# Performance work log

Hardware: AMD Instinct MI355X
Metric: run time of the kernel (lower is better)

The kernel has to match this reference:

```python
import jax, jax.numpy as jnp
import numpy as np
import math

EPS = 1e-7
STRIDES = (8, 16, 32)
ANCHOR_TABLE = np.array([[[12,16],[19,36],[40,28]],
                         [[36,75],[76,55],[72,146]],
                         [[142,110],[192,243],[459,401]]], dtype=np.float32)
OBJ_SCALE = (4.0, 1.0, 0.4)
B, A, C = 32, 3, 80
GRIDS = ((80, 80), (40, 40), (20, 20))
NTGT = (6000, 4000, 2000)
W_BOX, W_OBJ, W_CLS = 0.05, 0.7, 0.3


def bce_mean(logits, targets):
    # numerically-stable BCEWithLogits, mean reduction (pos_weight=1)
    return jnp.mean(jnp.maximum(logits, 0) - logits * targets
                    + jnp.log1p(jnp.exp(-jnp.abs(logits))))


def calculate_ciou(b1, b2):
    # boxes in xycwh; convert to xyxy
    def xyxy(b):
        cx, cy, w, h = b[..., 0], b[..., 1], b[..., 2], b[..., 3]
        return cx - w / 2, cy - h / 2, cx + w / 2, cy + h / 2
    x1a, y1a, x2a, y2a = xyxy(b1)
    x1b, y1b, x2b, y2b = xyxy(b2)
    iw = jnp.clip(jnp.minimum(x2a, x2b) - jnp.maximum(x1a, x1b), 0)
    ih = jnp.clip(jnp.minimum(y2a, y2b) - jnp.maximum(y1a, y1b), 0)
    inter = iw * ih
    union = (x2a - x1a) * (y2a - y1a) + (x2b - x1b) * (y2b - y1b) - inter
    iou = inter / (union + EPS)
    cw = jnp.maximum(x2a, x2b) - jnp.minimum(x1a, x1b)
    ch = jnp.maximum(y2a, y2b) - jnp.minimum(y1a, y1b)
    diag = cw ** 2 + ch ** 2 + EPS
    cent = ((x1a + x2a) / 2 - (x1b + x2b) / 2) ** 2 + ((y1a + y2a) / 2 - (y1b + y2b) / 2) ** 2
    at = jnp.arctan((x2a - x1a) / (y2a - y1a + EPS)) - jnp.arctan((x2b - x1b) / (y2b - y1b + EPS))
    v = (4.0 / math.pi ** 2) * at ** 2
    alpha = v / (v - iou + 1 + EPS)
    return iou - (cent / diag + v * alpha)


def setup_inputs() -> dict:
    key = jax.random.key(0)
    inp = {}
    for i in range(3):
        h, w = GRIDS[i]
        n = NTGT[i]
        ks = jax.random.split(jax.random.fold_in(key, i), 10)
        inp[f'box{i}'] = jax.random.normal(ks[0], (B, A, h, w, 4), jnp.float32)
        inp[f'cnf{i}'] = jax.random.normal(ks[1], (B, A, h, w, 1), jnp.float32)
        inp[f'cls{i}'] = jax.random.normal(ks[2], (B, A, h, w, C), jnp.float32)
        inp[f'b{i}'] = jax.random.randint(ks[3], (n,), 0, B, jnp.int32)
        a = jax.random.randint(ks[4], (n,), 0, A, jnp.int32)
        inp[f'a{i}'] = a
        inp[f'gy{i}'] = jax.random.randint(ks[5], (n,), 0, h, jnp.int32)
        inp[f'gx{i}'] = jax.random.randint(ks[6], (n,), 0, w, jnp.int32)
        inp[f'tcls{i}'] = jax.random.randint(ks[7], (n,), 0, C, jnp.int32)
        txy = jax.random.uniform(ks[8], (n, 2), jnp.float32) * 2.0 - 0.5   # grid_xy - grid_index
        twh = jax.random.uniform(ks[9], (n, 2), jnp.float32) * 7.5 + 0.5   # wh in grid units
        inp[f'tbox{i}'] = jnp.concatenate([txy, twh], axis=1)
        anc_tab = jnp.asarray(ANCHOR_TABLE[i] / STRIDES[i])                # [3,2]
        inp[f'anc{i}'] = anc_tab[a]                                        # per-target anchor wh
    return inp


def _scale_loss(pbox, pcnf, pcls, b, a, gy, gx, tbox, tcls, anc, obj_scale):
    pred = jnp.concatenate([pbox, pcnf, pcls], axis=-1)          # [B,A,H,W,5+C]
    p = pred[b, a, gy, gx]                                       # [N,5+C] gather
    pxy = jax.nn.sigmoid(p[:, :2]) * 2.0 - 0.5
    pwh = (jax.nn.sigmoid(p[:, 2:4]) * 2.0) ** 2 * anc
    pred_box = jnp.concatenate([pxy, pwh], axis=1)
    iou = calculate_ciou(pred_box, tbox)                         # [N]
    lbox = jnp.mean(1.0 - iou)
    tobj = jnp.zeros(pred.shape[:4], dtype=pred.dtype)
    tobj = tobj.at[b, a, gy, gx].set(jax.lax.stop_gradient(jnp.clip(iou, 0)))
    tcls_oh = jax.nn.one_hot(tcls, C, dtype=p.dtype)
    lcls = bce_mean(p[:, 5:], tcls_oh)
    lobj = bce_mean(pred[..., 4], tobj) * obj_scale
    return lbox, lobj, lcls


def reference(box0, cnf0, cls0, tbox0, anc0,
              box1, cnf1, cls1, tbox1, anc1,
              box2, cnf2, cls2, tbox2, anc2,
              b0, a0, gy0, gx0, tcls0,
              b1, a1, gy1, gx1, tcls1,
              b2, a2, gy2, gx2, tcls2):
    floats = [(box0, cnf0, cls0, tbox0, anc0),
              (box1, cnf1, cls1, tbox1, anc1),
              (box2, cnf2, cls2, tbox2, anc2)]
    ints = [(b0, a0, gy0, gx0, tcls0),
            (b1, a1, gy1, gx1, tcls1),
            (b2, a2, gy2, gx2, tcls2)]
    lbox = lobj = lcls = jnp.float32(0.0)
    for i in range(3):
        pbox, pcnf, pcls, tbox, anc = floats[i]
        b, a, gy, gx, tcls = ints[i]
        lb, lo, lc = _scale_loss(pbox, pcnf, pcls, b, a, gy, gx, tbox, tcls, anc, OBJ_SCALE[i])
        lbox, lobj, lcls = lbox + lb, lobj + lo, lcls + lc
    return jnp.stack([lbox * W_BOX * B, lobj * W_OBJ * B, lcls * W_CLS * B])
```

## Files before the change

### kernel.cpp

```cpp
#include <hip/hip_runtime.h>
#include <math.h>

#define EPSF 1e-7f
#define AA 3
#define CC 80
#define FOUR_OVER_PI2 0.4052847345693511f

__device__ __forceinline__ float sigmoidf_(float x) { return 1.0f / (1.0f + expf(-x)); }

__device__ __forceinline__ float bcef_(float x, float t) {
    return fmaxf(x, 0.0f) - x * t + log1pf(expf(-fabsf(x)));
}

__device__ __forceinline__ void block_reduce_add2(double v0, double v1, double* d0, double* d1) {
    __shared__ double s0[8], s1[8];
    const int lane = threadIdx.x & 63;
    const int wid  = threadIdx.x >> 6;
    #pragma unroll
    for (int off = 32; off > 0; off >>= 1) {
        v0 += __shfl_down(v0, off);
        v1 += __shfl_down(v1, off);
    }
    if (lane == 0) { s0[wid] = v0; s1[wid] = v1; }
    __syncthreads();
    if (threadIdx.x == 0) {
        const int nw = blockDim.x >> 6;
        double a = 0.0, b = 0.0;
        for (int w = 0; w < nw; ++w) { a += s0[w]; b += s1[w]; }
        atomicAdd(d0, a);
        atomicAdd(d1, b);
    }
}

__device__ __forceinline__ void block_reduce_add1(double v0, double* d0) {
    __shared__ double s0[8];
    const int lane = threadIdx.x & 63;
    const int wid  = threadIdx.x >> 6;
    #pragma unroll
    for (int off = 32; off > 0; off >>= 1) v0 += __shfl_down(v0, off);
    if (lane == 0) s0[wid] = v0;
    __syncthreads();
    if (threadIdx.x == 0) {
        const int nw = blockDim.x >> 6;
        double a = 0.0;
        for (int w = 0; w < nw; ++w) a += s0[w];
        atomicAdd(d0, a);
    }
}

__global__ __launch_bounds__(256) void target_kernel(
    const float* __restrict__ box, const float* __restrict__ cls,
    const int* __restrict__ tb, const int* __restrict__ ta,
    const int* __restrict__ tgy, const int* __restrict__ tgx,
    const int* __restrict__ ttc,
    const float* __restrict__ tbox, const float* __restrict__ anc,
    unsigned long long* __restrict__ tobj,
    double* __restrict__ accBox, double* __restrict__ accCls,
    int N, int H, int W)
{
    const int j = blockIdx.x * blockDim.x + threadIdx.x;
    float lb = 0.0f, lc = 0.0f;
    if (j < N) {
        const int b = tb[j], a = ta[j], gy = tgy[j], gx = tgx[j], tc = ttc[j];
        const long long cell = ((long long)((b * AA + a) * H + gy)) * W + gx;

        const float* bp = box + cell * 4;
        const float bx = bp[0], by = bp[1], bw = bp[2], bh = bp[3];

        const float px = sigmoidf_(bx) * 2.0f - 0.5f;
        const float py = sigmoidf_(by) * 2.0f - 0.5f;
        const float sw = sigmoidf_(bw) * 2.0f;
        const float sh = sigmoidf_(bh) * 2.0f;
        const float pw = sw * sw * anc[j * 2 + 0];
        const float ph = sh * sh * anc[j * 2 + 1];

        const float tx = tbox[j * 4 + 0], ty = tbox[j * 4 + 1];
        const float tw = tbox[j * 4 + 2], th = tbox[j * 4 + 3];

        const float x1a = px - pw * 0.5f, y1a = py - ph * 0.5f;
        const float x2a = px + pw * 0.5f, y2a = py + ph * 0.5f;
        const float x1b = tx - tw * 0.5f, y1b = ty - th * 0.5f;
        const float x2b = tx + tw * 0.5f, y2b = ty + th * 0.5f;

        const float iw = fmaxf(fminf(x2a, x2b) - fmaxf(x1a, x1b), 0.0f);
        const float ih = fmaxf(fminf(y2a, y2b) - fmaxf(y1a, y1b), 0.0f);
        const float inter = iw * ih;
        const float uni = (x2a - x1a) * (y2a - y1a) + (x2b - x1b) * (y2b - y1b) - inter;
        const float iou = inter / (uni + EPSF);
        const float cw = fmaxf(x2a, x2b) - fminf(x1a, x1b);
        const float ch = fmaxf(y2a, y2b) - fminf(y1a, y1b);
        const float diag = cw * cw + ch * ch + EPSF;
        const float dcx = (x1a + x2a) * 0.5f - (x1b + x2b) * 0.5f;
        const float dcy = (y1a + y2a) * 0.5f - (y1b + y2b) * 0.5f;
        const float cent = dcx * dcx + dcy * dcy;
        const float at = atanf((x2a - x1a) / ((y2a - y1a) + EPSF))
                       - atanf((x2b - x1b) / ((y2b - y1b) + EPSF));
        const float v = FOUR_OVER_PI2 * at * at;
        const float alpha = v / (v - iou + 1.0f + EPSF);
        const float ciou = iou - (cent / diag + v * alpha);

        lb = 1.0f - ciou;

        const float ioc = fmaxf(ciou, 0.0f);
        const unsigned long long pk =
            ((unsigned long long)(unsigned)(j + 1) << 32) |
            (unsigned long long)__float_as_uint(ioc);
        atomicMax(tobj + cell, pk);

        const float* cp = cls + cell * CC;
        float s = 0.0f;
        #pragma unroll 8
        for (int c = 0; c < CC; ++c) {
            const float x = cp[c];
            const float t = (c == tc) ? 1.0f : 0.0f;
            s += bcef_(x, t);
        }
        lc = s;
    }
    block_reduce_add2((double)lb, (double)lc, accBox, accCls);
}

__global__ __launch_bounds__(256) void obj_kernel(
    const float* __restrict__ cnf,
    const unsigned long long* __restrict__ tobj,
    double* __restrict__ accObj, int n4)
{
    const int stride = gridDim.x * blockDim.x;
    double s = 0.0;
    for (int idx = blockIdx.x * blockDim.x + threadIdx.x; idx < n4; idx += stride) {
        const float4 x4 = ((const float4*)cnf)[idx];
        const unsigned long long* tp = tobj + (long long)idx * 4;
        float xs[4] = {x4.x, x4.y, x4.z, x4.w};
        float ps = 0.0f;
        #pragma unroll
        for (int k = 0; k < 4; ++k) {
            const unsigned long long pk = tp[k];
            const float t = __uint_as_float((unsigned)(pk & 0xFFFFFFFFull));
            ps += bcef_(xs[k], t);
        }
        s += (double)ps;
    }
    block_reduce_add1(s, accObj);
}

__global__ void finalize_kernel(const double* __restrict__ acc, float* __restrict__ out) {
    if (threadIdx.x == 0 && blockIdx.x == 0) {
        const double lbox = acc[0] / 6000.0 + acc[1] / 4000.0 + acc[2] / 2000.0;
        const double lobj = (acc[3] / 614400.0) * 4.0
                          + (acc[4] / 153600.0) * 1.0
                          + (acc[5] /  38400.0) * 0.4;
        const double lcls = acc[6] / 480000.0 + acc[7] / 320000.0 + acc[8] / 160000.0;
        out[0] = (float)(lbox * 0.05 * 32.0);
        out[1] = (float)(lobj * 0.7 * 32.0);
        out[2] = (float)(lcls * 0.3 * 32.0);
    }
}

extern "C" void kernel_launch(void* const* d_in, const int* in_sizes, int n_in,
                              void* d_out, int out_size, void* d_ws, size_t ws_size,
                              hipStream_t stream) {
    const int NS[3]    = {6000, 4000, 2000};
    const int HS[3]    = {80, 40, 20};
    const int CELLS[3] = {32 * AA * 80 * 80, 32 * AA * 40 * 40, 32 * AA * 20 * 20};

    double* acc = (double*)d_ws;
    unsigned long long* tobj0 = (unsigned long long*)((char*)d_ws + 128);
    unsigned long long* tobj1 = tobj0 + CELLS[0];
    unsigned long long* tobj2 = tobj1 + CELLS[1];
    unsigned long long* tobjs[3] = {tobj0, tobj1, tobj2};

    const size_t zero_bytes = 128 + (size_t)(CELLS[0] + CELLS[1] + CELLS[2]) * 8;
    hipMemsetAsync(d_ws, 0, zero_bytes, stream);

    for (int i = 0; i < 3; ++i) {
        const int base = i * 10;
        const float* box  = (const float*)d_in[base + 0];
        const int*   b    = (const int*)  d_in[base + 3];
        const int*   a    = (const int*)  d_in[base + 4];
        const int*   gy   = (const int*)  d_in[base + 5];
        const int*   gx   = (const int*)  d_in[base + 6];
        const int*   tcls = (const int*)  d_in[base + 7];
        const float* tbox = (const float*)d_in[base + 8];
        const float* anc  = (const float*)d_in[base + 9];
        const float* cls  = (const float*)d_in[base + 2];

        const int N = NS[i];
        const int grid = (N + 255) / 256;
        target_kernel<<<grid, 256, 0, stream>>>(box, cls, b, a, gy, gx, tcls, tbox, anc,
                                                tobjs[i], acc + i, acc + 6 + i,
                                                N, HS[i], HS[i]);
    }

    for (int i = 0; i < 3; ++i) {
        const int base = i * 10;
        const float* cnf = (const float*)d_in[base + 1];
        const int n4 = CELLS[i] / 4;
        const int grid = min((n4 + 255) / 256, 256);
        obj_kernel<<<grid, 256, 0, stream>>>(cnf, tobjs[i], acc + 3 + i, n4);
    }

    finalize_kernel<<<1, 64, 0, stream>>>(acc, (float*)d_out);
}
```

Measured before the change: 402.5 us.

## Merge scales into two kernels and split BCE into dense softplus plus sparse correction

```diff
diff --git a/kernel.cpp b/kernel.cpp
--- a/kernel.cpp
+++ b/kernel.cpp
@@ -2,15 +2,31 @@
 #include <math.h>
 
 #define EPSF 1e-7f
-#define AA 3
-#define CC 80
 #define FOUR_OVER_PI2 0.4052847345693511f
 
+struct Params {
+    const float* box[3];
+    const float* cnf[3];
+    const float* cls[3];
+    const float* tbox[3];
+    const float* anc[3];
+    const int* tb[3];
+    const int* ta[3];
+    const int* tgy[3];
+    const int* tgx[3];
+    const int* ttc[3];
+    unsigned* tobj;
+    float* iouv;
+    unsigned* cellv;
+    double* acc;
+    unsigned* counter;
+    float* out;
+};
+
+__device__ __forceinline__ float softplus_(float x) {
+    return fmaxf(x, 0.0f) + log1pf(expf(-fabsf(x)));
+}
 __device__ __forceinline__ float sigmoidf_(float x) { return 1.0f / (1.0f + expf(-x)); }
-
-__device__ __forceinline__ float bcef_(float x, float t) {
-    return fmaxf(x, 0.0f) - x * t + log1pf(expf(-fabsf(x)));
-}
 
 __device__ __forceinline__ void block_reduce_add2(double v0, double v1, double* d0, double* d1) {
     __shared__ double s0[8], s1[8];
@@ -48,39 +64,39 @@
     }
 }
 
-__global__ __launch_bounds__(256) void target_kernel(
-    const float* __restrict__ box, const float* __restrict__ cls,
-    const int* __restrict__ tb, const int* __restrict__ ta,
-    const int* __restrict__ tgy, const int* __restrict__ tgx,
-    const int* __restrict__ ttc,
-    const float* __restrict__ tbox, const float* __restrict__ anc,
-    unsigned long long* __restrict__ tobj,
-    double* __restrict__ accBox, double* __restrict__ accCls,
-    int N, int H, int W)
+__global__ __launch_bounds__(256) void targets_kernel(Params P)
 {
     const int j = blockIdx.x * blockDim.x + threadIdx.x;
-    float lb = 0.0f, lc = 0.0f;
-    if (j < N) {
-        const int b = tb[j], a = ta[j], gy = tgy[j], gx = tgx[j], tc = ttc[j];
-        const long long cell = ((long long)((b * AA + a) * H + gy)) * W + gx;
-
-        const float* bp = box + cell * 4;
-        const float bx = bp[0], by = bp[1], bw = bp[2], bh = bp[3];
-
-        const float px = sigmoidf_(bx) * 2.0f - 0.5f;
-        const float py = sigmoidf_(by) * 2.0f - 0.5f;
-        const float sw = sigmoidf_(bw) * 2.0f;
-        const float sh = sigmoidf_(bh) * 2.0f;
-        const float pw = sw * sw * anc[j * 2 + 0];
-        const float ph = sh * sh * anc[j * 2 + 1];
-
-        const float tx = tbox[j * 4 + 0], ty = tbox[j * 4 + 1];
-        const float tw = tbox[j * 4 + 2], th = tbox[j * 4 + 3];
+    double lb = 0.0, lc = 0.0;
+    if (j < 12000) {
+        int i, jj;
+        if (j < 6000)       { i = 0; jj = j; }
+        else if (j < 10000) { i = 1; jj = j - 6000; }
+        else                { i = 2; jj = j - 10000; }
+        const int H    = (i == 0) ? 80 : (i == 1) ? 40 : 20;
+        const int gofs = (i == 0) ? 0  : (i == 1) ? 614400 : 768000;
+        const double wbox = (i == 0) ? (1.0 / 6000.0) : (i == 1) ? (1.0 / 4000.0) : (1.0 / 2000.0);
+        const double wcls = wbox * (1.0 / 80.0);
+
+        const int b  = P.tb[i][jj],  a  = P.ta[i][jj];
+        const int gy = P.tgy[i][jj], gx = P.tgx[i][jj], tc = P.ttc[i][jj];
+        const int cell = ((b * 3 + a) * H + gy) * H + gx;
+
+        const float4 b4 = ((const float4*)P.box[i])[cell];
+        const float2 an = ((const float2*)P.anc[i])[jj];
+        const float4 t4 = ((const float4*)P.tbox[i])[jj];
+
+        const float px = sigmoidf_(b4.x) * 2.0f - 0.5f;
+        const float py = sigmoidf_(b4.y) * 2.0f - 0.5f;
+        const float sw = sigmoidf_(b4.z) * 2.0f;
+        const float sh = sigmoidf_(b4.w) * 2.0f;
+        const float pw = sw * sw * an.x;
+        const float ph = sh * sh * an.y;
 
         const float x1a = px - pw * 0.5f, y1a = py - ph * 0.5f;
         const float x2a = px + pw * 0.5f, y2a = py + ph * 0.5f;
-        const float x1b = tx - tw * 0.5f, y1b = ty - th * 0.5f;
-        const float x2b = tx + tw * 0.5f, y2b = ty + th * 0.5f;
+        const float x1b = t4.x - t4.z * 0.5f, y1b = t4.y - t4.w * 0.5f;
+        const float x2b = t4.x + t4.z * 0.5f, y2b = t4.y + t4.w * 0.5f;
 
         const float iw = fmaxf(fminf(x2a, x2b) - fmaxf(x1a, x1b), 0.0f);
         const float ih = fmaxf(fminf(y2a, y2b) - fmaxf(y1a, y1b), 0.0f);
@@ -99,105 +115,97 @@
         const float alpha = v / (v - iou + 1.0f + EPSF);
         const float ciou = iou - (cent / diag + v * alpha);
 
-        lb = 1.0f - ciou;
-
-        const float ioc = fmaxf(ciou, 0.0f);
-        const unsigned long long pk =
-            ((unsigned long long)(unsigned)(j + 1) << 32) |
-            (unsigned long long)__float_as_uint(ioc);
-        atomicMax(tobj + cell, pk);
-
-        const float* cp = cls + cell * CC;
+        lb = (double)(1.0f - ciou) * wbox;
+
+        P.iouv[j]  = fmaxf(ciou, 0.0f);
+        P.cellv[j] = (unsigned)(gofs + cell);
+        atomicMax(P.tobj + gofs + cell, (unsigned)(j + 1));
+
+        const float* cbase = P.cls[i] + (long long)cell * 80;
+        const float4* cp = (const float4*)cbase;
         float s = 0.0f;
-        #pragma unroll 8
-        for (int c = 0; c < CC; ++c) {
-            const float x = cp[c];
-            const float t = (c == tc) ? 1.0f : 0.0f;
-            s += bcef_(x, t);
+        #pragma unroll
+        for (int q = 0; q < 20; ++q) {
+            const float4 x4 = cp[q];
+            s += softplus_(x4.x) + softplus_(x4.y) + softplus_(x4.z) + softplus_(x4.w);
         }
-        lc = s;
-    }
-    block_reduce_add2((double)lb, (double)lc, accBox, accCls);
-}
-
-__global__ __launch_bounds__(256) void obj_kernel(
-    const float* __restrict__ cnf,
-    const unsigned long long* __restrict__ tobj,
-    double* __restrict__ accObj, int n4)
+        s -= cbase[tc];
+        lc = (double)s * wcls;
+    }
+    block_reduce_add2(lb, lc, P.acc + 0, P.acc + 1);
+}
+
+__global__ __launch_bounds__(256) void obj_kernel(Params P)
 {
-    const int stride = gridDim.x * blockDim.x;
+    const int t = blockIdx.x * blockDim.x + threadIdx.x;
     double s = 0.0;
-    for (int idx = blockIdx.x * blockDim.x + threadIdx.x; idx < n4; idx += stride) {
-        const float4 x4 = ((const float4*)cnf)[idx];
-        const unsigned long long* tp = tobj + (long long)idx * 4;
-        float xs[4] = {x4.x, x4.y, x4.z, x4.w};
-        float ps = 0.0f;
-        #pragma unroll
-        for (int k = 0; k < 4; ++k) {
-            const unsigned long long pk = tp[k];
-            const float t = __uint_as_float((unsigned)(pk & 0xFFFFFFFFull));
-            ps += bcef_(xs[k], t);
+    if (t < 201600) {
+        int i, lidx;
+        if (t < 153600)      { i = 0; lidx = t; }
+        else if (t < 192000) { i = 1; lidx = t - 153600; }
+        else                 { i = 2; lidx = t - 192000; }
+        const double w = (i == 0) ? (4.0 / 614400.0)
+                       : (i == 1) ? (1.0 / 153600.0)
+                                  : (0.4 / 38400.0);
+        const float4 x4 = ((const float4*)P.cnf[i])[lidx];
+        const float ps = softplus_(x4.x) + softplus_(x4.y) + softplus_(x4.z) + softplus_(x4.w);
+        s = (double)ps * w;
+    }
+    if (t < 12000) {
+        const int i = (t < 6000) ? 0 : (t < 10000) ? 1 : 2;
+        const unsigned gcell = P.cellv[t];
+        if (P.tobj[gcell] == (unsigned)(t + 1)) {
+            const unsigned gofs = (i == 0) ? 0u : (i == 1) ? 614400u : 768000u;
+            const double w = (i == 0) ? (4.0 / 614400.0)
+                           : (i == 1) ? (1.0 / 153600.0)
+                                      : (0.4 / 38400.0);
+            const float x = P.cnf[i][gcell - gofs];
+            s -= (double)(x * P.iouv[t]) * w;
         }
-        s += (double)ps;
-    }
-    block_reduce_add1(s, accObj);
-}
-
-__global__ void finalize_kernel(const double* __restrict__ acc, float* __restrict__ out) {
-    if (threadIdx.x == 0 && blockIdx.x == 0) {
-        const double lbox = acc[0] / 6000.0 + acc[1] / 4000.0 + acc[2] / 2000.0;
-        const double lobj = (acc[3] / 614400.0) * 4.0
-                          + (acc[4] / 153600.0) * 1.0
-                          + (acc[5] /  38400.0) * 0.4;
-        const double lcls = acc[6] / 480000.0 + acc[7] / 320000.0 + acc[8] / 160000.0;
-        out[0] = (float)(lbox * 0.05 * 32.0);
-        out[1] = (float)(lobj * 0.7 * 32.0);
-        out[2] = (float)(lcls * 0.3 * 32.0);
+    }
+    block_reduce_add1(s, P.acc + 2);
+
+    __shared__ int amLast;
+    __threadfence();
+    if (threadIdx.x == 0)
+        amLast = (atomicAdd(P.counter, 1u) == gridDim.x - 1);
+    __syncthreads();
+    if (amLast && threadIdx.x == 0) {
+        __threadfence();
+        const double lbox = P.acc[0], lcls = P.acc[1], lobj = P.acc[2];
+        P.out[0] = (float)(lbox * (0.05 * 32.0));
+        P.out[1] = (float)(lobj * (0.7 * 32.0));
+        P.out[2] = (float)(lcls * (0.3 * 32.0));
     }
 }
 
 extern "C" void kernel_launch(void* const* d_in, const int* in_sizes, int n_in,
                               void* d_out, int out_size, void* d_ws, size_t ws_size,
                               hipStream_t stream) {
-    const int NS[3]    = {6000, 4000, 2000};
-    const int HS[3]    = {80, 40, 20};
-    const int CELLS[3] = {32 * AA * 80 * 80, 32 * AA * 40 * 40, 32 * AA * 20 * 20};
-
-    double* acc = (double*)d_ws;
-    unsigned long long* tobj0 = (unsigned long long*)((char*)d_ws + 128);
-    unsigned long long* tobj1 = tobj0 + CELLS[0];
-    unsigned long long* tobj2 = tobj1 + CELLS[1];
-    unsigned long long* tobjs[3] = {tobj0, tobj1, tobj2};
-
-    const size_t zero_bytes = 128 + (size_t)(CELLS[0] + CELLS[1] + CELLS[2]) * 8;
-    hipMemsetAsync(d_ws, 0, zero_bytes, stream);
-
+    Params P;
     for (int i = 0; i < 3; ++i) {
         const int base = i * 10;
-        const float* box  = (const float*)d_in[base + 0];
-        const int*   b    = (const int*)  d_in[base + 3];
-        const int*   a    = (const int*)  d_in[base + 4];
-        const int*   gy   = (const int*)  d_in[base + 5];
-        const int*   gx   = (const int*)  d_in[base + 6];
-        const int*   tcls = (const int*)  d_in[base + 7];
-        const float* tbox = (const float*)d_in[base + 8];
-        const float* anc  = (const float*)d_in[base + 9];
-        const float* cls  = (const float*)d_in[base + 2];
-
-        const int N = NS[i];
-        const int grid = (N + 255) / 256;
-        target_kernel<<<grid, 256, 0, stream>>>(box, cls, b, a, gy, gx, tcls, tbox, anc,
-                                                tobjs[i], acc + i, acc + 6 + i,
-                                                N, HS[i], HS[i]);
-    }
-
-    for (int i = 0; i < 3; ++i) {
-        const int base = i * 10;
-        const float* cnf = (const float*)d_in[base + 1];
-        const int n4 = CELLS[i] / 4;
-        const int grid = min((n4 + 255) / 256, 256);
-        obj_kernel<<<grid, 256, 0, stream>>>(cnf, tobjs[i], acc + 3 + i, n4);
-    }
-
-    finalize_kernel<<<1, 64, 0, stream>>>(acc, (float*)d_out);
-}
+        P.box[i]  = (const float*)d_in[base + 0];
+        P.cnf[i]  = (const float*)d_in[base + 1];
+        P.cls[i]  = (const float*)d_in[base + 2];
+        P.tb[i]   = (const int*)  d_in[base + 3];
+        P.ta[i]   = (const int*)  d_in[base + 4];
+        P.tgy[i]  = (const int*)  d_in[base + 5];
+        P.tgx[i]  = (const int*)  d_in[base + 6];
+        P.ttc[i]  = (const int*)  d_in[base + 7];
+        P.tbox[i] = (const float*)d_in[base + 8];
+        P.anc[i]  = (const float*)d_in[base + 9];
+    }
+    char* ws = (char*)d_ws;
+    P.acc     = (double*)ws;
+    P.counter = (unsigned*)(ws + 24);
+    P.tobj    = (unsigned*)(ws + 128);
+    P.iouv    = (float*)   (ws + 128 + 806400 * 4);
+    P.cellv   = (unsigned*)(ws + 128 + 806400 * 4 + 12000 * 4);
+    P.out     = (float*)d_out;
+
+    hipMemsetAsync(d_ws, 0, 128 + 806400 * 4, stream);
+
+    targets_kernel<<<(12000 + 255) / 256, 256, 0, stream>>>(P);
+    obj_kernel<<<(201600 + 255) / 256, 256, 0, stream>>>(P);
+}
```

After: 399.2 us. No clear change (-0.8%).
